# Performance work log

Hardware: AMD Instinct MI355X
Metric: run time of the kernel (lower is better)

The kernel has to match this reference:

```python
import jax, jax.numpy as jnp
import numpy as np

D_MODEL = 1024
H = 16
D_K = D_MODEL // H
B = 2
S = 2048


def setup_inputs() -> dict:
    key = jax.random.key(0)
    ks = jax.random.split(key, 11)
    scale = 1.0 / np.sqrt(D_MODEL)
    inp = {
        "query": jax.random.normal(ks[0], (B, S, D_MODEL), jnp.float32),
        "key_in": jax.random.normal(ks[1], (B, S, D_MODEL), jnp.float32),
        "value": jax.random.normal(ks[2], (B, S, D_MODEL), jnp.float32),
        # causal mask, broadcast over heads: 1 = keep, 0 = masked
        "mask": jnp.tril(jnp.ones((S, S), jnp.int32))[None, None, :, :].repeat(B, axis=0),
        "w_q": jax.random.normal(ks[3], (D_MODEL, D_MODEL), jnp.float32) * scale,
        "b_q": jax.random.normal(ks[4], (D_MODEL,), jnp.float32) * 0.01,
        "w_k": jax.random.normal(ks[5], (D_MODEL, D_MODEL), jnp.float32) * scale,
        "b_k": jax.random.normal(ks[6], (D_MODEL,), jnp.float32) * 0.01,
        "w_v": jax.random.normal(ks[7], (D_MODEL, D_MODEL), jnp.float32) * scale,
        "b_v": jax.random.normal(ks[8], (D_MODEL,), jnp.float32) * 0.01,
        "w_out": jax.random.normal(ks[9], (D_MODEL, D_MODEL), jnp.float32) * scale,
        "b_out": jax.random.normal(ks[10], (D_MODEL,), jnp.float32) * 0.01,
    }
    return inp


def _split_heads(x):
    # [B,S,D] -> [B,H,S,d_k]
    b, s, _ = x.shape
    return x.reshape(b, s, H, D_K).transpose(0, 2, 1, 3)


def reference(query, key_in, value, mask, w_q, b_q, w_k, b_k, w_v, b_v, w_out, b_out):
    q = _split_heads(query @ w_q.T + b_q)
    k = _split_heads(key_in @ w_k.T + b_k)
    v = _split_heads(value @ w_v.T + b_v)
    scores = jnp.einsum("bhqd,bhkd->bhqk", q, k) / jnp.sqrt(jnp.float32(D_K))
    scores = jnp.where(mask == 0, jnp.float32(-1e9), scores)
    attn = jax.nn.softmax(scores, axis=-1)  # dropout rate 0.0 -> identity
    out = jnp.einsum("bhqk,bhkd->bhqd", attn, v)
    out = out.transpose(0, 2, 1, 3).reshape(query.shape[0], -1, D_MODEL)
    return out @ w_out.T + b_out
```

## Files before the change

### kernel.cpp

```cpp
#include <hip/hip_runtime.h>
#include <hip/hip_bf16.h>

#define D_MODEL 1024
#define NH 16
#define DKH 64
#define BB 2
#define SS 2048
#define MTOT (BB * SS)

typedef __hip_bfloat16 bf16;
typedef __attribute__((ext_vector_type(8))) short short8;
typedef __attribute__((ext_vector_type(4))) short short4v;
typedef __attribute__((ext_vector_type(4))) float floatx4;

__device__ __forceinline__ bf16 f2bf(float x) { return __float2bfloat16(x); }

__device__ __forceinline__ void async_cp16(const void* g, void* l) {
  __builtin_amdgcn_global_load_lds(
      (const __attribute__((address_space(1))) unsigned int*)g,
      (__attribute__((address_space(3))) unsigned int*)l, 16, 0, 0);
}

__global__ __launch_bounds__(256) void convert_w_kernel(
    const float* __restrict__ wq, const float* __restrict__ wk,
    const float* __restrict__ wv, const float* __restrict__ wo,
    bf16* __restrict__ out) {
  const int id = blockIdx.x * 256 + threadIdx.x;
  const int m = id >> 18;
  const int loc = id & 262143;
  const float* src = (m == 0) ? wq : (m == 1) ? wk : (m == 2) ? wv : wo;
  const float4 v = *(const float4*)(src + (size_t)loc * 4);
  short4v s;
  bf16* pb = (bf16*)&s;
  pb[0] = f2bf(v.x); pb[1] = f2bf(v.y); pb[2] = f2bf(v.z); pb[3] = f2bf(v.w);
  *(short4v*)(out + ((size_t)m << 20) + (size_t)loc * 4) = s;
}

__device__ __forceinline__ void gemm_qkv_body(const float* __restrict__ A,
                                              const bf16* __restrict__ W,
                                              const float* __restrict__ Bi,
                                              bf16* __restrict__ C, int mode) {
  constexpr int N = 1024, K = 1024;
  __shared__ bf16 As[2][128 * 32];
  __shared__ bf16 Ws[2][128 * 32];

  const int tid = threadIdx.x;
  const int w = tid >> 6, lane = tid & 63, quad = lane >> 4, n16 = lane & 15;
  const int bx = blockIdx.x;
  const int bm = bx & 31, bn = bx >> 5;
  const int wm = (w & 1) * 64, wn = (w >> 1) * 64;

  const int ra = tid >> 3, ca = tid & 7;
  const int rb = lane >> 2, cb = lane & 3;

  const float* Af = A + (size_t)(bm * 128) * K;
  const bf16* Wg0 = W + (size_t)(bn * 128) * K;

  float4 pa4[4];
  auto loadA = [&](int kk) {
#pragma unroll
    for (int ii = 0; ii < 4; ii++)
      pa4[ii] = *(const float4*)(Af + (size_t)(ii * 32 + ra) * K + kk + ca * 4);
  };
  auto stageA = [&](int buf) {
#pragma unroll
    for (int ii = 0; ii < 4; ii++) {
      short4v s;
      bf16* pb = (bf16*)&s;
      pb[0] = f2bf(pa4[ii].x); pb[1] = f2bf(pa4[ii].y);
      pb[2] = f2bf(pa4[ii].z); pb[3] = f2bf(pa4[ii].w);
      *(short4v*)(&As[buf][(ii * 32 + ra) * 32 + ca * 4]) = s;
    }
  };
  auto issueW = [&](int buf, int kk) {
    const bf16* Wg = Wg0 + kk;
#pragma unroll
    for (int ii = 0; ii < 2; ii++) {
      const int R = w * 32 + ii * 16 + rb;
      async_cp16(Wg + (size_t)R * K + cb * 8,
                 (void*)&Ws[buf][(w * 32 + ii * 16) * 32]);
    }
  };

  floatx4 acc[4][4] = {};
  loadA(0);
  issueW(0, 0);
  int buf = 0;
  for (int k0 = 0; k0 < K; k0 += 32) {
    stageA(buf);
    __syncthreads();
    if (k0 + 32 < K) { loadA(k0 + 32); issueW(buf ^ 1, k0 + 32); }

    short8 af[4], bfr[4];
#pragma unroll
    for (int i = 0; i < 4; i++)
      af[i] = *(const short8*)(&As[buf][(wm + i * 16 + n16) * 32 + quad * 8]);
#pragma unroll
    for (int j = 0; j < 4; j++)
      bfr[j] = *(const short8*)(&Ws[buf][(wn + j * 16 + n16) * 32 + quad * 8]);
#pragma unroll
    for (int i = 0; i < 4; i++)
#pragma unroll
      for (int j = 0; j < 4; j++)
        acc[i][j] = __builtin_amdgcn_mfma_f32_16x16x32_bf16(af[i], bfr[j], acc[i][j], 0, 0, 0);
    buf ^= 1;
  }

  float bv[4];
#pragma unroll
  for (int j = 0; j < 4; j++) bv[j] = Bi[bn * 128 + wn + j * 16 + n16];

#pragma unroll
  for (int i = 0; i < 4; i++) {
    const int rowb = bm * 128 + wm + i * 16 + quad * 4;
#pragma unroll
    for (int j = 0; j < 4; j++) {
      const int col = bn * 128 + wn + j * 16 + n16;
      if (mode == 1) {
        short4v s;
        bf16* pb = (bf16*)&s;
#pragma unroll
        for (int r = 0; r < 4; r++) pb[r] = f2bf(acc[i][j][r] + bv[j]);
        *(short4v*)(C + (size_t)col * MTOT + rowb) = s;
      } else {
#pragma unroll
        for (int r = 0; r < 4; r++)
          C[(size_t)(rowb + r) * N + col] = f2bf(acc[i][j][r] + bv[j]);
      }
    }
  }
}

__global__ __launch_bounds__(256) void gemm_qkv_kernel(
    const float* __restrict__ q_in, const float* __restrict__ k_in,
    const float* __restrict__ v_in, const bf16* __restrict__ Wb,
    const float* __restrict__ bq, const float* __restrict__ bk,
    const float* __restrict__ bv, bf16* __restrict__ Qw,
    bf16* __restrict__ Kw, bf16* __restrict__ VTw) {
  const int z = blockIdx.z;
  const float* A = (z == 0) ? q_in : (z == 1) ? k_in : v_in;
  const bf16* W = Wb + ((size_t)z << 20);
  const float* Bi = (z == 0) ? bq : (z == 1) ? bk : bv;
  bf16* C = (z == 0) ? Qw : (z == 1) ? Kw : VTw;
  gemm_qkv_body(A, W, Bi, C, (z == 2) ? 1 : 0);
}

__global__ __launch_bounds__(256) void gemm_out_kernel(
    const bf16* __restrict__ A, const bf16* __restrict__ W,
    const float* __restrict__ Bi, float* __restrict__ C) {
  constexpr int N = 1024, K = 1024;
  __shared__ bf16 As[2][64 * 32];
  __shared__ bf16 Ws[2][128 * 32];

  const int tid = threadIdx.x;
  const int w = tid >> 6, lane = tid & 63, quad = lane >> 4, n16 = lane & 15;
  const int bx = blockIdx.x;
  const int bm = bx & 63, bn = bx >> 6;
  const int wm = (w & 1) * 32, wn = (w >> 1) * 64;

  const int rl = lane >> 2, cl = lane & 3;

  const bf16* Ag0 = A + (size_t)(bm * 64) * K;
  const bf16* Wg0 = W + (size_t)(bn * 128) * K;

  auto issue = [&](int buf, int kk) {
    async_cp16(Ag0 + (size_t)(w * 16 + rl) * K + kk + cl * 8,
               (void*)&As[buf][(w * 16) * 32]);
    const bf16* Wg = Wg0 + kk;
#pragma unroll
    for (int ii = 0; ii < 2; ii++) {
      const int R = w * 32 + ii * 16 + rl;
      async_cp16(Wg + (size_t)R * K + cl * 8,
                 (void*)&Ws[buf][(w * 32 + ii * 16) * 32]);
    }
  };

  floatx4 acc[2][4] = {};
  issue(0, 0);
  int buf = 0;
  for (int k0 = 0; k0 < K; k0 += 32) {
    __syncthreads();
    if (k0 + 32 < K) issue(buf ^ 1, k0 + 32);

    short8 af[2], bfr[4];
#pragma unroll
    for (int i = 0; i < 2; i++)
      af[i] = *(const short8*)(&As[buf][(wm + i * 16 + n16) * 32 + quad * 8]);
#pragma unroll
    for (int j = 0; j < 4; j++)
      bfr[j] = *(const short8*)(&Ws[buf][(wn + j * 16 + n16) * 32 + quad * 8]);
#pragma unroll
    for (int i = 0; i < 2; i++)
#pragma unroll
      for (int j = 0; j < 4; j++)
        acc[i][j] = __builtin_amdgcn_mfma_f32_16x16x32_bf16(af[i], bfr[j], acc[i][j], 0, 0, 0);
    buf ^= 1;
  }

  float bv[4];
#pragma unroll
  for (int j = 0; j < 4; j++) bv[j] = Bi[bn * 128 + wn + j * 16 + n16];

#pragma unroll
  for (int i = 0; i < 2; i++) {
    const int rowb = bm * 64 + wm + i * 16 + quad * 4;
#pragma unroll
    for (int j = 0; j < 4; j++) {
      const int col = bn * 128 + wn + j * 16 + n16;
#pragma unroll
      for (int r = 0; r < 4; r++)
        C[(size_t)(rowb + r) * N + col] = acc[i][j][r] + bv[j];
    }
  }
}

__global__ __launch_bounds__(256) void attn_kernel(const bf16* __restrict__ Q,
                                                   const bf16* __restrict__ Kg,
                                                   const bf16* __restrict__ VT,
                                                   bf16* __restrict__ O) {
  constexpr int BN = 128, LDK = 72, LDV = 136, LDP = 136;
  __shared__ bf16 Ks[128 * LDK];
  __shared__ bf16 Vs[64 * LDV];
  __shared__ bf16 Pw[4 * 16 * LDP];

  const int tid = threadIdx.x;
  const int w = tid >> 6, lane = tid & 63, quad = lane >> 4, n16 = lane & 15;
  const int hb = blockIdx.x;
  const int h = hb & 15, b = hb >> 4, p = blockIdx.y;
  const size_t qoff = (size_t)b * SS * D_MODEL + h * DKH;
  const bf16* VTh = VT + (size_t)(h * DKH) * MTOT + (size_t)b * SS;

  const int kvr = tid >> 3, ck = tid & 7;
  const int dd = tid >> 4, cv = tid & 15;

  short8 kreg[4], vreg[4];
  auto loadKV = [&](int kv0) {
#pragma unroll
    for (int ii = 0; ii < 4; ii++) {
      kreg[ii] = *(const short8*)(Kg + qoff + (size_t)(kv0 + ii * 32 + kvr) * D_MODEL + ck * 8);
      vreg[ii] = *(const short8*)(VTh + (size_t)(ii * 16 + dd) * MTOT + kv0 + cv * 8);
    }
  };

  for (int hf = 0; hf < 2; hf++) {
    const int q0 = (hf == 0) ? p * 64 : (31 - p) * 64;
    const int q0w = q0 + w * 16;
    const int nt = (q0 + 191) >> 7;

    short8 aQ0, aQ1;
    {
      const bf16* qp = Q + qoff + (size_t)(q0w + n16) * D_MODEL + quad * 8;
      aQ0 = *(const short8*)(qp);
      aQ1 = *(const short8*)(qp + 32);
    }

    floatx4 facc[4] = {};
    float m_i[4], l_i[4];
#pragma unroll
    for (int r = 0; r < 4; r++) { m_i[r] = -1e30f; l_i[r] = 0.f; }

    loadKV(0);
    for (int t = 0; t < nt; t++) {
#pragma unroll
      for (int ii = 0; ii < 4; ii++) {
        *(short8*)(&Ks[(ii * 32 + kvr) * LDK + ck * 8]) = kreg[ii];
        *(short8*)(&Vs[(ii * 16 + dd) * LDV + cv * 8]) = vreg[ii];
      }
      __syncthreads();
      if (t + 1 < nt) loadKV((t + 1) * BN);

      const int kv0 = t * BN;
      float pv[8][4];
      float mt[4] = {-1e30f, -1e30f, -1e30f, -1e30f};
      const int qrow_base = q0w + quad * 4;
#pragma unroll
      for (int blk = 0; blk < 8; blk++) {
        floatx4 z = {};
        short8 bk0 = *(const short8*)(&Ks[(blk * 16 + n16) * LDK + quad * 8]);
        short8 bk1 = *(const short8*)(&Ks[(blk * 16 + n16) * LDK + 32 + quad * 8]);
        z = __builtin_amdgcn_mfma_f32_16x16x32_bf16(aQ0, bk0, z, 0, 0, 0);
        z = __builtin_amdgcn_mfma_f32_16x16x32_bf16(aQ1, bk1, z, 0, 0, 0);
        const int kvg = kv0 + blk * 16 + n16;
#pragma unroll
        for (int r = 0; r < 4; r++) {
          float s = z[r] * 0.125f;
          if (kvg > qrow_base + r) s = -1e30f;
          pv[blk][r] = s;
          mt[r] = fmaxf(mt[r], s);
        }
      }
#pragma unroll
      for (int off = 1; off < 16; off <<= 1)
#pragma unroll
        for (int r = 0; r < 4; r++) mt[r] = fmaxf(mt[r], __shfl_xor(mt[r], off, 64));

      float alpha[4];
#pragma unroll
      for (int r = 0; r < 4; r++) {
        const float mn = fmaxf(m_i[r], mt[r]);
        alpha[r] = __expf(m_i[r] - mn);
        m_i[r] = mn;
      }
      float rs[4] = {0.f, 0.f, 0.f, 0.f};
#pragma unroll
      for (int blk = 0; blk < 8; blk++)
#pragma unroll
        for (int r = 0; r < 4; r++) {
          const float pe = __expf(pv[blk][r] - m_i[r]);
          pv[blk][r] = pe;
          rs[r] += pe;
        }
#pragma unroll
      for (int off = 1; off < 16; off <<= 1)
#pragma unroll
        for (int r = 0; r < 4; r++) rs[r] += __shfl_xor(rs[r], off, 64);
#pragma unroll
      for (int r = 0; r < 4; r++) l_i[r] = l_i[r] * alpha[r] + rs[r];
#pragma unroll
      for (int d = 0; d < 4; d++)
#pragma unroll
        for (int r = 0; r < 4; r++) facc[d][r] *= alpha[r];

      bf16* pw = &Pw[w * 16 * LDP];
#pragma unroll
      for (int blk = 0; blk < 8; blk++)
#pragma unroll
        for (int r = 0; r < 4; r++)
          pw[(quad * 4 + r) * LDP + blk * 16 + n16] = f2bf(pv[blk][r]);

      short8 aP[4];
#pragma unroll
      for (int c = 0; c < 4; c++)
        aP[c] = *(const short8*)(&pw[n16 * LDP + c * 32 + quad * 8]);

#pragma unroll
      for (int d = 0; d < 4; d++)
#pragma unroll
        for (int c = 0; c < 4; c++) {
          short8 bvf = *(const short8*)(&Vs[(d * 16 + n16) * LDV + c * 32 + quad * 8]);
          facc[d] = __builtin_amdgcn_mfma_f32_16x16x32_bf16(aP[c], bvf, facc[d], 0, 0, 0);
        }
      __syncthreads();
    }

#pragma unroll
    for (int r = 0; r < 4; r++) {
      const float inv = 1.f / l_i[r];
      const int qrow = q0w + quad * 4 + r;
      bf16* op = O + qoff + (size_t)qrow * D_MODEL;
#pragma unroll
      for (int d = 0; d < 4; d++) op[d * 16 + n16] = f2bf(facc[d][r] * inv);
    }
  }
}

extern "C" void kernel_launch(void* const* d_in, const int* in_sizes, int n_in,
                              void* d_out, int out_size, void* d_ws, size_t ws_size,
                              hipStream_t stream) {
  (void)in_sizes; (void)n_in; (void)out_size; (void)ws_size;
  const float* query  = (const float*)d_in[0];
  const float* key_in = (const float*)d_in[1];
  const float* value  = (const float*)d_in[2];
  const float* w_q = (const float*)d_in[4];
  const float* b_q = (const float*)d_in[5];
  const float* w_k = (const float*)d_in[6];
  const float* b_k = (const float*)d_in[7];
  const float* w_v = (const float*)d_in[8];
  const float* b_v = (const float*)d_in[9];
  const float* w_o = (const float*)d_in[10];
  const float* b_o = (const float*)d_in[11];
  float* outp = (float*)d_out;

  const size_t mat = (size_t)MTOT * D_MODEL;
  bf16* Qws  = (bf16*)d_ws;
  bf16* Kws  = Qws + mat;
  bf16* VTws = Kws + mat;
  bf16* Wb   = VTws + mat;

  convert_w_kernel<<<4096, 256, 0, stream>>>(w_q, w_k, w_v, w_o, Wb);

  dim3 gq(256, 1, 3);
  gemm_qkv_kernel<<<gq, 256, 0, stream>>>(query, key_in, value, Wb, b_q, b_k,
                                          b_v, Qws, Kws, VTws);
  dim3 ga(NH * BB, 16);
  attn_kernel<<<ga, 256, 0, stream>>>(Qws, Kws, VTws, Qws);
  gemm_out_kernel<<<512, 256, 0, stream>>>(Qws, Wb + ((size_t)3 << 20), b_o, outp);
}
```

Before: 275.7 us.

## Double GEMM K-tile to 64 and XOR-swizzle LDS layouts for projection GEMMs

Both the QKV projection GEMM and the output GEMM move from a 32-wide to a 64-wide K tile, which halves the number of barrier-separated iterations. Each iteration now runs two MFMA sub-steps. Shared-memory tiles now use an XOR swizzle on 16-byte chunks (chunk ^ row&7), applied on both the async global-to-LDS writes and the fragment reads, to avoid LDS bank conflicts. The A-load mapping is also reorganised so each thread loads 32 contiguous floats per row. The cost is double the LDS footprint per block and more registers for the A prefetch, which may reduce occupancy.

```diff
diff --git a/kernel.cpp b/kernel.cpp
--- a/kernel.cpp
+++ b/kernel.cpp
@@ -40,9 +40,9 @@
                                               const bf16* __restrict__ W,
                                               const float* __restrict__ Bi,
                                               bf16* __restrict__ C, int mode) {
-  constexpr int N = 1024, K = 1024;
-  __shared__ bf16 As[2][128 * 32];
-  __shared__ bf16 Ws[2][128 * 32];
+  constexpr int N = 1024, K = 1024, BK = 64;
+  __shared__ bf16 As[2][128 * BK];
+  __shared__ bf16 Ws[2][128 * BK];
 
   const int tid = threadIdx.x;
   const int w = tid >> 6, lane = tid & 63, quad = lane >> 4, n16 = lane & 15;
@@ -50,35 +50,34 @@
   const int bm = bx & 31, bn = bx >> 5;
   const int wm = (w & 1) * 64, wn = (w >> 1) * 64;
 
-  const int ra = tid >> 3, ca = tid & 7;
-  const int rb = lane >> 2, cb = lane & 3;
-
-  const float* Af = A + (size_t)(bm * 128) * K;
+  const int arow = tid >> 1, ahalf = tid & 1;
+  const float* Af = A + (size_t)(bm * 128 + arow) * K + ahalf * 32;
+  const int wr = lane >> 3, wc = lane & 7;
   const bf16* Wg0 = W + (size_t)(bn * 128) * K;
 
-  float4 pa4[4];
+  float4 pa[8];
   auto loadA = [&](int kk) {
 #pragma unroll
-    for (int ii = 0; ii < 4; ii++)
-      pa4[ii] = *(const float4*)(Af + (size_t)(ii * 32 + ra) * K + kk + ca * 4);
+    for (int j = 0; j < 8; j++) pa[j] = *(const float4*)(Af + kk + j * 4);
   };
   auto stageA = [&](int buf) {
 #pragma unroll
-    for (int ii = 0; ii < 4; ii++) {
-      short4v s;
-      bf16* pb = (bf16*)&s;
-      pb[0] = f2bf(pa4[ii].x); pb[1] = f2bf(pa4[ii].y);
-      pb[2] = f2bf(pa4[ii].z); pb[3] = f2bf(pa4[ii].w);
-      *(short4v*)(&As[buf][(ii * 32 + ra) * 32 + ca * 4]) = s;
+    for (int j = 0; j < 4; j++) {
+      short8 s8;
+      bf16* pb = (bf16*)&s8;
+      const float4 a = pa[2 * j], b = pa[2 * j + 1];
+      pb[0] = f2bf(a.x); pb[1] = f2bf(a.y); pb[2] = f2bf(a.z); pb[3] = f2bf(a.w);
+      pb[4] = f2bf(b.x); pb[5] = f2bf(b.y); pb[6] = f2bf(b.z); pb[7] = f2bf(b.w);
+      const int chunk = (ahalf * 4 + j) ^ (arow & 7);
+      *(short8*)(&As[buf][arow * BK + chunk * 8]) = s8;
     }
   };
   auto issueW = [&](int buf, int kk) {
-    const bf16* Wg = Wg0 + kk;
-#pragma unroll
-    for (int ii = 0; ii < 2; ii++) {
-      const int R = w * 32 + ii * 16 + rb;
-      async_cp16(Wg + (size_t)R * K + cb * 8,
-                 (void*)&Ws[buf][(w * 32 + ii * 16) * 32]);
+#pragma unroll
+    for (int ii = 0; ii < 4; ii++) {
+      const int R = w * 32 + ii * 8 + wr;
+      async_cp16(Wg0 + (size_t)R * K + kk + ((wc ^ (R & 7)) * 8),
+                 (void*)&Ws[buf][(w * 32 + ii * 8) * BK]);
     }
   };
 
@@ -86,23 +85,30 @@
   loadA(0);
   issueW(0, 0);
   int buf = 0;
-  for (int k0 = 0; k0 < K; k0 += 32) {
+  for (int k0 = 0; k0 < K; k0 += BK) {
     stageA(buf);
     __syncthreads();
-    if (k0 + 32 < K) { loadA(k0 + 32); issueW(buf ^ 1, k0 + 32); }
-
-    short8 af[4], bfr[4];
-#pragma unroll
-    for (int i = 0; i < 4; i++)
-      af[i] = *(const short8*)(&As[buf][(wm + i * 16 + n16) * 32 + quad * 8]);
-#pragma unroll
-    for (int j = 0; j < 4; j++)
-      bfr[j] = *(const short8*)(&Ws[buf][(wn + j * 16 + n16) * 32 + quad * 8]);
-#pragma unroll
-    for (int i = 0; i < 4; i++)
-#pragma unroll
-      for (int j = 0; j < 4; j++)
-        acc[i][j] = __builtin_amdgcn_mfma_f32_16x16x32_bf16(af[i], bfr[j], acc[i][j], 0, 0, 0);
+    if (k0 + BK < K) { loadA(k0 + BK); issueW(buf ^ 1, k0 + BK); }
+
+#pragma unroll
+    for (int s = 0; s < 2; s++) {
+      short8 af[4], bfr[4];
+#pragma unroll
+      for (int i = 0; i < 4; i++) {
+        const int R = wm + i * 16 + n16;
+        af[i] = *(const short8*)(&As[buf][R * BK + (((s * 4 + quad) ^ (R & 7)) * 8)]);
+      }
+#pragma unroll
+      for (int j = 0; j < 4; j++) {
+        const int R = wn + j * 16 + n16;
+        bfr[j] = *(const short8*)(&Ws[buf][R * BK + (((s * 4 + quad) ^ (R & 7)) * 8)]);
+      }
+#pragma unroll
+      for (int i = 0; i < 4; i++)
+#pragma unroll
+        for (int j = 0; j < 4; j++)
+          acc[i][j] = __builtin_amdgcn_mfma_f32_16x16x32_bf16(af[i], bfr[j], acc[i][j], 0, 0, 0);
+    }
     buf ^= 1;
   }
 
@@ -148,9 +154,9 @@
 __global__ __launch_bounds__(256) void gemm_out_kernel(
     const bf16* __restrict__ A, const bf16* __restrict__ W,
     const float* __restrict__ Bi, float* __restrict__ C) {
-  constexpr int N = 1024, K = 1024;
-  __shared__ bf16 As[2][64 * 32];
-  __shared__ bf16 Ws[2][128 * 32];
+  constexpr int N = 1024, K = 1024, BK = 64;
+  __shared__ bf16 As[2][64 * BK];
+  __shared__ bf16 Ws[2][128 * BK];
 
   const int tid = threadIdx.x;
   const int w = tid >> 6, lane = tid & 63, quad = lane >> 4, n16 = lane & 15;
@@ -158,42 +164,52 @@
   const int bm = bx & 63, bn = bx >> 6;
   const int wm = (w & 1) * 32, wn = (w >> 1) * 64;
 
-  const int rl = lane >> 2, cl = lane & 3;
+  const int wr = lane >> 3, wc = lane & 7;
 
   const bf16* Ag0 = A + (size_t)(bm * 64) * K;
   const bf16* Wg0 = W + (size_t)(bn * 128) * K;
 
   auto issue = [&](int buf, int kk) {
-    async_cp16(Ag0 + (size_t)(w * 16 + rl) * K + kk + cl * 8,
-               (void*)&As[buf][(w * 16) * 32]);
-    const bf16* Wg = Wg0 + kk;
 #pragma unroll
     for (int ii = 0; ii < 2; ii++) {
-      const int R = w * 32 + ii * 16 + rl;
-      async_cp16(Wg + (size_t)R * K + cl * 8,
-                 (void*)&Ws[buf][(w * 32 + ii * 16) * 32]);
+      const int R = w * 16 + ii * 8 + wr;
+      async_cp16(Ag0 + (size_t)R * K + kk + ((wc ^ (R & 7)) * 8),
+                 (void*)&As[buf][(w * 16 + ii * 8) * BK]);
+    }
+#pragma unroll
+    for (int ii = 0; ii < 4; ii++) {
+      const int R = w * 32 + ii * 8 + wr;
+      async_cp16(Wg0 + (size_t)R * K + kk + ((wc ^ (R & 7)) * 8),
+                 (void*)&Ws[buf][(w * 32 + ii * 8) * BK]);
     }
   };
 
   floatx4 acc[2][4] = {};
   issue(0, 0);
   int buf = 0;
-  for (int k0 = 0; k0 < K; k0 += 32) {
+  for (int k0 = 0; k0 < K; k0 += BK) {
     __syncthreads();
-    if (k0 + 32 < K) issue(buf ^ 1, k0 + 32);
-
-    short8 af[2], bfr[4];
-#pragma unroll
-    for (int i = 0; i < 2; i++)
-      af[i] = *(const short8*)(&As[buf][(wm + i * 16 + n16) * 32 + quad * 8]);
-#pragma unroll
-    for (int j = 0; j < 4; j++)
-      bfr[j] = *(const short8*)(&Ws[buf][(wn + j * 16 + n16) * 32 + quad * 8]);
-#pragma unroll
-    for (int i = 0; i < 2; i++)
-#pragma unroll
-      for (int j = 0; j < 4; j++)
-        acc[i][j] = __builtin_amdgcn_mfma_f32_16x16x32_bf16(af[i], bfr[j], acc[i][j], 0, 0, 0);
+    if (k0 + BK < K) issue(buf ^ 1, k0 + BK);
+
+#pragma unroll
+    for (int s = 0; s < 2; s++) {
+      short8 af[2], bfr[4];
+#pragma unroll
+      for (int i = 0; i < 2; i++) {
+        const int R = wm + i * 16 + n16;
+        af[i] = *(const short8*)(&As[buf][R * BK + (((s * 4 + quad) ^ (R & 7)) * 8)]);
+      }
+#pragma unroll
+      for (int j = 0; j < 4; j++) {
+        const int R = wn + j * 16 + n16;
+        bfr[j] = *(const short8*)(&Ws[buf][R * BK + (((s * 4 + quad) ^ (R & 7)) * 8)]);
+      }
+#pragma unroll
+      for (int i = 0; i < 2; i++)
+#pragma unroll
+        for (int j = 0; j < 4; j++)
+          acc[i][j] = __builtin_amdgcn_mfma_f32_16x16x32_bf16(af[i], bfr[j], acc[i][j], 0, 0, 0);
+    }
     buf ^= 1;
   }
 
```

After: 297.0 us. 1.08x slower.
